# Performance work log

Measured on AMD Instinct MI355X. Metric: run time of the kernel, lower is better.

Reference implementation:

```python
import jax, jax.numpy as jnp
import numpy as np

KERNEL = 10   # kernel_size (asserted == 10 in the original)
HEADS = 4
BN_SCALE = 1.0 / np.sqrt(1.0 + 1e-5)  # eval-mode BatchNorm1d (running mean 0, var 1, affine 1/0)


def get_dct_matrix(N):
    k = np.arange(N)[:, None].astype(np.float64)
    i = np.arange(N)[None, :].astype(np.float64)
    w = np.full((N, 1), np.sqrt(2.0 / N))
    w[0, 0] = np.sqrt(1.0 / N)
    dct_m = w * np.cos(np.pi * (i + 0.5) * k / N)
    idct_m = np.linalg.inv(dct_m)
    return dct_m.astype(np.float32), idct_m.astype(np.float32)


def conv1d(x, w):  # x [B,C,L], w [O,I,K], valid, no bias
    return jax.lax.conv_general_dilated(x, w, (1,), 'VALID',
                                        dimension_numbers=('NCH', 'OIH', 'NCH'))


def conv_stack(x, w1, w2):  # Conv1d(k=6) -> ReLU -> Conv1d(k=5) -> ReLU
    return jax.nn.relu(conv1d(jax.nn.relu(conv1d(x, w1)), w2))


# vmap over the 4 heads' weights -> [H,B,D,L]
heads_conv = jax.vmap(conv_stack, in_axes=(None, 0, 0))


def _forward(src, cq1, cq2, ck1, ck2, lw, lb, giw, gia, gib, gbw, gba, gbb,
             gow, goa, gob, dct_n, output_n, input_n):
    bs, in_feat = src.shape[0], src.shape[2]
    src = src[:, :input_n]                                   # [B,50,48]
    src_key = jnp.swapaxes(src, 1, 2)[:, :, :input_n - output_n]  # [B,48,25]
    src_query = jnp.swapaxes(src, 1, 2)[:, :, -KERNEL:]           # [B,48,10]

    dct_np, idct_np = get_dct_matrix(KERNEL + output_n)
    dct_m = jnp.asarray(dct_np)
    idct_m = jnp.asarray(idct_np)

    vn = input_n - KERNEL - output_n + 1  # 16 overlapping value windows
    vl = KERNEL + output_n                # window length 35
    idx = np.arange(vl)[None, :] + np.arange(vn)[:, None]    # [16,35]
    windows = src[:, idx]                                    # [B,16,35,48]
    # DCT per window then flatten per-joint coeffs: [B,16,48*dct_n]
    val = jnp.einsum('dv,bnvf->bndf', dct_m[:dct_n], windows)
    src_value = jnp.swapaxes(val, 2, 3).reshape(bs, vn, -1)  # [B,16,480]

    key_h = heads_conv(src_key / 1000.0, ck1, ck2)           # [H,B,512,16]
    query_h = heads_conv(src_query / 1000.0, cq1, cq2)       # [H,B,512,1]

    # sum-normalized (non-softmax) attention
    score = jnp.einsum('hbdq,hbdk->hbqk', query_h, key_h) + 1e-15  # [H,B,1,16]
    att_w = score / jnp.sum(score, axis=3, keepdims=True)
    dct_att = jnp.einsum('hbk,bkf->hbf', att_w[:, :, 0], src_value)  # [H,B,480]
    dct_att = dct_att.reshape(HEADS, bs, in_feat, dct_n)
    att_cat = jnp.transpose(dct_att, (1, 0, 2, 3)).reshape(bs, HEADS * in_feat, dct_n)
    # Linear over the concatenated head/joint axis: [B,48,dct_n]
    att_lin = jnp.einsum('bmd,nm->bnd', att_cat, lw) + lb[None, :, None]

    # last kernel_size frames + last frame repeated output_n times
    gather_idx = np.concatenate([np.arange(input_n - KERNEL, input_n),
                                 np.full(output_n, input_n - 1)])
    input_gcn = src[:, gather_idx]                           # [B,35,48]
    dct_in = jnp.einsum('dv,bvf->bfd', dct_m[:dct_n], input_gcn)  # [B,48,10]
    dct_in = jnp.concatenate([dct_in, att_lin], axis=-1)     # [B,48,20]

    # GCN (Mao et al. style): learnable adjacency [48,48], eval-mode BN, tanh
    def gc(h, a, w, b):
        return jnp.einsum('nm,bmf->bnf', a, h @ w) + b

    y = jnp.tanh(gc(dct_in, gia, giw, gib) * BN_SCALE)       # [B,48,512]
    for s in range(gbw.shape[0]):
        r = y
        for j in range(2):
            y = jnp.tanh(gc(y, gba[s, j], gbw[s, j], gbb[s, j]) * BN_SCALE)
        y = y + r
    dct_out = gc(y, goa, gow, gob) + dct_in                  # [B,48,20]

    out_gcn = jnp.einsum('vd,bnd->bvn', idct_m[:, :dct_n], dct_out[:, :, :dct_n])  # [B,35,48]
    return out_gcn[:, :, None, :]                            # [B,35,itera=1,48]


def setup_inputs() -> dict:
    key = jax.random.key(0)
    ks = jax.random.split(key, 16)
    bs, in_feat, d_model, dct_n = 256, 48, 512, 10
    s = 0.05
    return {
        'src': jax.random.normal(ks[0], (bs, 50, in_feat), jnp.float32) * 1000.0,
        'convQ_w1': jax.random.normal(ks[1], (HEADS, d_model, in_feat, 6), jnp.float32) * s,
        'convQ_w2': jax.random.normal(ks[2], (HEADS, d_model, d_model, 5), jnp.float32) * s,
        'convK_w1': jax.random.normal(ks[3], (HEADS, d_model, in_feat, 6), jnp.float32) * s,
        'convK_w2': jax.random.normal(ks[4], (HEADS, d_model, d_model, 5), jnp.float32) * s,
        'linear_w': jax.random.normal(ks[5], (in_feat, HEADS * in_feat), jnp.float32) * s,
        'linear_b': jax.random.normal(ks[6], (in_feat,), jnp.float32) * s,
        'gc_in_w': jax.random.normal(ks[7], (2 * dct_n, d_model), jnp.float32) * s,
        'gc_in_att': jax.random.normal(ks[8], (in_feat, in_feat), jnp.float32) * s,
        'gc_in_b': jax.random.normal(ks[9], (d_model,), jnp.float32) * s,
        'gcb_w': jax.random.normal(ks[10], (2, 2, d_model, d_model), jnp.float32) * s,
        'gcb_att': jax.random.normal(ks[11], (2, 2, in_feat, in_feat), jnp.float32) * s,
        'gcb_b': jax.random.normal(ks[12], (2, 2, d_model), jnp.float32) * s,
        'gc_out_w': jax.random.normal(ks[13], (d_model, 2 * dct_n), jnp.float32) * s,
        'gc_out_att': jax.random.normal(ks[14], (in_feat, in_feat), jnp.float32) * s,
        'gc_out_b': jax.random.normal(ks[15], (2 * dct_n,), jnp.float32) * s,
        'dct_n': 10, 'output_n': 25, 'input_n': 50, 'itera': 1,
    }


def reference(src, convQ_w1, convQ_w2, convK_w1, convK_w2, linear_w, linear_b,
              gc_in_w, gc_in_att, gc_in_b, gcb_w, gcb_att, gcb_b,
              gc_out_w, gc_out_att, gc_out_b, dct_n, output_n, input_n, itera):
    # itera=1 path only (itera>1 in the original references undefined attrs)
    return _forward(src, convQ_w1, convQ_w2, convK_w1, convK_w2, linear_w, linear_b,
                    gc_in_w, gc_in_att, gc_in_b, gcb_w, gcb_att, gcb_b,
                    gc_out_w, gc_out_att, gc_out_b, dct_n, output_n, input_n)
```

## Files before the change

kernel.cpp:

```cpp
#include <hip/hip_runtime.h>
#include <math.h>

static constexpr float BN_SCALE_F = 0.9999950000374997f;

typedef __bf16 bf16;
typedef bf16 bf16x8 __attribute__((ext_vector_type(8)));
typedef bf16 bf16x4 __attribute__((ext_vector_type(4)));
typedef float floatx4 __attribute__((ext_vector_type(4)));

#define GLOBAL_AS __attribute__((address_space(1)))
#define LDS_AS __attribute__((address_space(3)))

__device__ __forceinline__ float tanh_fast(float x) {
    const float e = __expf(2.f * x);
    return 1.f - 2.f / (e + 1.f);
}

__device__ __forceinline__ void d_trw1(int id, const float* w, bf16* wt) {
    if (id < 4 * 512 * 320) {
        int ho = id / 320, c = id % 320;
        float v = (c < 288) ? w[(long)ho * 288 + (c % 48) * 6 + (c / 48)] * 1e-3f : 0.f;
        wt[id] = (bf16)v;
    }
}
__global__ __launch_bounds__(256) void k_prep(
    const float* __restrict__ src, const float* __restrict__ cq1,
    const float* __restrict__ ck1, const float* __restrict__ cq2,
    const float* __restrict__ ck2, const float* __restrict__ gbw,
    const float* __restrict__ giw, const float* __restrict__ gow,
    const float* __restrict__ gba, float* __restrict__ dct10,
    bf16* __restrict__ srcbf, bf16* __restrict__ w1tq, bf16* __restrict__ w1tk,
    bf16* __restrict__ w2tq, bf16* __restrict__ w2tk, bf16* __restrict__ gbwF,
    bf16* __restrict__ giwF, bf16* __restrict__ gowT, bf16* __restrict__ gbaP) {
    __shared__ float lds[4160];
    int bb = blockIdx.x;
    const int t = threadIdx.x;
    if (bb < 2) {
        int id = bb * 256 + t;
        if (id < 350) {
            int k = id / 35, i = id % 35;
            double w = (k == 0) ? sqrt(1.0 / 35.0) : sqrt(2.0 / 35.0);
            dct10[id] = (float)(w * cos(3.14159265358979323846 * (i + 0.5) * k / 35.0));
        }
        return;
    }
    bb -= 2;
    if (bb < 2401) {
        int id = bb * 256 + t;
        if (id < 614656) srcbf[id] = (bf16)(id < 614400 ? src[id] : 0.f);
        return;
    }
    bb -= 2401;
    if (bb < 2560) { d_trw1(bb * 256 + t, cq1, w1tq); return; }
    bb -= 2560;
    if (bb < 2560) { d_trw1(bb * 256 + t, ck1, w1tk); return; }
    bb -= 2560;
    if (bb < 4096) {
        const bool isQ = bb < 2048;
        const int ho = isQ ? bb : bb - 2048;
        const float* wrow = (isQ ? cq2 : ck2) + (long)ho * 2560;
        bf16* orow = (isQ ? w2tq : w2tk) + (long)ho * 2560;
        for (int j = t; j < 2560; j += 256) lds[j] = wrow[j];
        __syncthreads();
        for (int c = t; c < 2560; c += 256) {
            const int k = c >> 9, ii = c & 511;
            orow[c] = (bf16)lds[ii * 5 + k];
        }
        return;
    }
    bb -= 4096;
    if (bb < 256) {
        const int l = bb >> 6, tile = bb & 63;
        const int tr = tile >> 3, tc = tile & 7;
        const float* in = gbw + (long)l * 262144;
        bf16* o = gbwF + (long)l * 262144;
#pragma unroll
        for (int r = 0; r < 16; ++r) {
            const int kl = (t >> 6) * 16 + r, ml = t & 63;
            lds[kl * 65 + ml] = in[(long)(tr * 64 + kl) * 512 + tc * 64 + ml];
        }
        __syncthreads();
        for (int j = t; j < 4096; j += 256) {
            const int q = j >> 9, r4 = j & 511;
            const int gl = q >> 2, sl = (q >> 1) & 1, jt = q & 1;
            const int lane = r4 >> 3, e = r4 & 7;
            const int fr = lane & 15, fq = lane >> 4;
            const int kk = sl * 32 + fq * 8 + e;
            const int ff = gl * 32 + jt * 16 + fr;
            o[(long)(tc * 2 + gl) * 16384 + (long)(tr * 2 + sl) * 1024 + jt * 512 + r4] =
                (bf16)lds[kk * 65 + ff];
        }
        return;
    }
    bb -= 256;
    if (bb < 128) {
        int id = bb * 256 + t;
        if (id < 32768) {
            const int r2 = id & 2047;
            const int s = r2 >> 10, r3 = r2 & 1023;
            const int jt = r3 >> 9, r4 = r3 & 511;
            const int lane = r4 >> 3, e = r4 & 7;
            const int fr = lane & 15, fq = lane >> 4;
            const int g = id >> 11;
            const int k = s * 32 + fq * 8 + e;
            const int f = g * 32 + jt * 16 + fr;
            giwF[id] = (bf16)(k < 20 ? giw[k * 512 + f] : 0.f);
        }
        return;
    }
    bb -= 128;
    if (bb < 64) {
        int id = bb * 256 + t;
        int d = id >> 9, k = id & 511;
        gowT[id] = (bf16)(d < 20 ? gow[k * 20 + d] : 0.f);
        return;
    }
    bb -= 64;
    {
        int id = bb * 256 + t;
        if (id < 12288) {
            int l = id / 3072, r = id % 3072, n = r >> 6, m = r & 63;
            gbaP[id] = (bf16)(m < 48 ? gba[l * 2304 + n * 48 + m] : 0.f);
        }
    }
}

__global__ __launch_bounds__(256) void k_conv1(
    const bf16* __restrict__ w1tk, const bf16* __restrict__ w1tq,
    const bf16* __restrict__ srcbf, bf16* __restrict__ r1k,
    bf16* __restrict__ r1q) {
    int bx, by, bz;
    const bf16* A;
    bf16* C;
    int NT, toff;
    long cStr;
    {
        const int i = blockIdx.x;
        if (i < 1280) {
            bz = i / 320;
            const int r = i % 320;
            bx = r % 40;
            by = r / 40;
            A = w1tk; C = r1k; NT = 20; toff = 0; cStr = 2621440L;
        } else {
            const int j = i - 1280;
            bz = j / 80;
            const int r = j % 80;
            bx = r % 10;
            by = r / 10;
            A = w1tq; C = r1q; NT = 5; toff = 40; cStr = 655360L;
        }
    }
    __shared__ bf16 As[64 * 64];
    __shared__ bf16 Bs[128 * 64];
    const int tid = threadIdx.x;
    const int wave = tid >> 6;
    const int lane = tid & 63;
    const int wm = (wave & 1) * 32;
    const int wn = (wave >> 1) * 64;
    const int m0 = by * 64;
    const int n0 = bx * 128;
    A += (long)bz * (512L * 320);

    const int srow = lane >> 3;
    const int gch = (lane & 7) ^ srow;
    const bf16* aptr[2];
    const bf16* bptr[4];
#pragma unroll
    for (int i = 0; i < 2; ++i) {
        const int ar = wave * 16 + i * 8 + srow;
        aptr[i] = A + (long)(m0 + ar) * 320 + gch * 8;
    }
#pragma unroll
    for (int i = 0; i < 4; ++i) {
        const int ar = wave * 32 + i * 8 + srow;
        const int n = n0 + ar;
        const long bbase = (long)(n / NT) * 2400 + (long)((n % NT) + toff) * 48;
        bptr[i] = srcbf + bbase + gch * 8;
    }

    floatx4 acc[4][2];
#pragma unroll
    for (int j = 0; j < 4; ++j)
#pragma unroll
        for (int i = 0; i < 2; ++i) acc[j][i] = (floatx4){0.f, 0.f, 0.f, 0.f};

    const int fr = lane & 15;
    const int fq = lane >> 4;
    const int fx = lane & 7;

    for (int k0 = 0; k0 < 320; k0 += 64) {
#pragma unroll
        for (int i = 0; i < 2; ++i)
            __builtin_amdgcn_global_load_lds(
                (const GLOBAL_AS void*)(aptr[i] + k0),
                (LDS_AS void*)(As + (wave * 16 + i * 8) * 64), 16, 0, 0);
#pragma unroll
        for (int i = 0; i < 4; ++i)
            __builtin_amdgcn_global_load_lds(
                (const GLOBAL_AS void*)(bptr[i] + k0),
                (LDS_AS void*)(Bs + (wave * 32 + i * 8) * 64), 16, 0, 0);
        __syncthreads();
#pragma unroll
        for (int kk = 0; kk < 2; ++kk) {
            bf16x8 af[2], bfr[4];
#pragma unroll
            for (int im = 0; im < 2; ++im)
                af[im] = *(const bf16x8*)(As + (wm + im * 16 + fr) * 64 +
                                          ((((kk << 2) + fq) ^ fx) << 3));
#pragma unroll
            for (int in = 0; in < 4; ++in)
                bfr[in] = *(const bf16x8*)(Bs + (wn + in * 16 + fr) * 64 +
                                           ((((kk << 2) + fq) ^ fx) << 3));
#pragma unroll
            for (int in = 0; in < 4; ++in)
#pragma unroll
                for (int im = 0; im < 2; ++im)
                    acc[in][im] = __builtin_amdgcn_mfma_f32_16x16x32_bf16(
                        af[im], bfr[in], acc[in][im], 0, 0, 0);
        }
        __syncthreads();
    }
#pragma unroll
    for (int in = 0; in < 4; ++in) {
        const long n = n0 + wn + in * 16 + fr;
#pragma unroll
        for (int im = 0; im < 2; ++im) {
            floatx4 v = acc[in][im];
            const long m = m0 + wm + im * 16 + (fq << 2);
            v.x = fmaxf(v.x, 0.f);
            v.y = fmaxf(v.y, 0.f);
            v.z = fmaxf(v.z, 0.f);
            v.w = fmaxf(v.w, 0.f);
            bf16* Cp = C + (long)bz * cStr + n * 512 + m;
            bf16x4 ov;
            ov[0] = (bf16)v.x;
            ov[1] = (bf16)v.y;
            ov[2] = (bf16)v.z;
            ov[3] = (bf16)v.w;
            *(bf16x4*)Cp = ov;
        }
    }
}

__global__ __launch_bounds__(256) void k_conv2(
    const bf16* __restrict__ w2tk, const bf16* __restrict__ r1k,
    bf16* __restrict__ keyh, const bf16* __restrict__ w2tq,
    const bf16* __restrict__ r1q, bf16* __restrict__ qh) {
    const int K = 2560;
    int bx, by, bz;
    const bf16 *A, *B;
    bf16* C;
    bool kMode;
    long aStr, bStr, cStr;
    {
        const int i = blockIdx.x;
        if (i < 1024) {
            const int slot = i & 7;
            bz = slot >> 1;
            const int half = slot & 1;
            const int j = i >> 3;
            bx = half * 16 + (j & 15);
            by = j >> 4;
            A = w2tk; B = r1k; C = keyh; kMode = true;
            aStr = 512L * 2560; bStr = 2621440L; cStr = 2097152L;
        } else {
            const int j = i - 1024;
            bz = j >> 4;
            const int r = j & 15;
            bx = r & 1;
            by = r >> 1;
            A = w2tq; B = r1q; C = qh; kMode = false;
            aStr = 512L * 2560; bStr = 655360L; cStr = 131072L;
        }
    }
    __shared__ bf16 As[64 * 64];
    __shared__ bf16 Bs[160 * 64];
    const int tid = threadIdx.x;
    const int wave = tid >> 6;
    const int lane = tid & 63;
    const int wm = (wave & 1) * 32;
    const int wn = (wave >> 1) * 64;
    const int m0 = by * 64;
    const int n0 = bx * 128;
    A += (long)bz * aStr;
    B += (long)bz * bStr;

    const int srow = lane >> 3;
    const int gch = (lane & 7) ^ srow;
    const bf16* aptr[2];
#pragma unroll
    for (int i = 0; i < 2; ++i) {
        const int ar = wave * 16 + i * 8 + srow;
        aptr[i] = A + (long)(m0 + ar) * K + gch * 8;
    }

    floatx4 acc[4][2];
#pragma unroll
    for (int j = 0; j < 4; ++j)
#pragma unroll
        for (int i = 0; i < 2; ++i) acc[j][i] = (floatx4){0.f, 0.f, 0.f, 0.f};

    const int fr = lane & 15;
    const int fq = lane >> 4;
    const int fx = lane & 7;

    if (kMode) {
        const bf16* bptrK[5];
        int ldsBK[5];
#pragma unroll
        for (int j = 0; j < 5; ++j) {
            const int rloc = wave * 40 + j * 8 + srow;
            const int brel = rloc / 20, pos = rloc % 20;
            bptrK[j] = B + ((long)((bx * 8 + brel) * 20 + pos)) * 512 +
                       ((lane & 7) ^ (pos & 7)) * 8;
            ldsBK[j] = rloc * 64 + (lane & 7) * 8;
        }
        const int bq = wn >> 4;
        for (int c0i = 0; c0i < 8; ++c0i) {
            const int c0 = c0i * 64;
#pragma unroll
            for (int w = 0; w < 5; ++w) {
                const int k0 = w * 512 + c0;
#pragma unroll
                for (int i = 0; i < 2; ++i)
                    __builtin_amdgcn_global_load_lds(
                        (const GLOBAL_AS void*)(aptr[i] + k0),
                        (LDS_AS void*)(As + (wave * 16 + i * 8) * 64), 16, 0, 0);
                if (w == 0) {
#pragma unroll
                    for (int j = 0; j < 5; ++j)
                        __builtin_amdgcn_global_load_lds(
                            (const GLOBAL_AS void*)(bptrK[j] + c0),
                            (LDS_AS void*)(Bs + ldsBK[j]), 16, 0, 0);
                }
                __syncthreads();
#pragma unroll
                for (int kk = 0; kk < 2; ++kk) {
                    bf16x8 af[2], bfr[4];
#pragma unroll
                    for (int im = 0; im < 2; ++im)
                        af[im] = *(const bf16x8*)(As + (wm + im * 16 + fr) * 64 +
                                                  ((((kk << 2) + fq) ^ fx) << 3));
#pragma unroll
                    for (int nt = 0; nt < 4; ++nt) {
                        const int row = (bq + nt) * 20 + fr + w;
                        bfr[nt] = *(const bf16x8*)(
                            Bs + row * 64 +
                            ((((kk << 2) + fq) ^ ((fr + w) & 7)) << 3));
                    }
#pragma unroll
                    for (int nt = 0; nt < 4; ++nt)
#pragma unroll
                        for (int im = 0; im < 2; ++im)
                            acc[nt][im] = __builtin_amdgcn_mfma_f32_16x16x32_bf16(
                                af[im], bfr[nt], acc[nt][im], 0, 0, 0);
                }
                __syncthreads();
            }
        }
    } else {
        const bf16* bptr[4];
#pragma unroll
        for (int i = 0; i < 4; ++i) {
            const int ar = wave * 32 + i * 8 + srow;
            bptr[i] = B + (long)(n0 + ar) * K + gch * 8;
        }
        for (int k0 = 0; k0 < K; k0 += 64) {
#pragma unroll
            for (int i = 0; i < 2; ++i)
                __builtin_amdgcn_global_load_lds(
                    (const GLOBAL_AS void*)(aptr[i] + k0),
                    (LDS_AS void*)(As + (wave * 16 + i * 8) * 64), 16, 0, 0);
#pragma unroll
            for (int i = 0; i < 4; ++i)
                __builtin_amdgcn_global_load_lds(
                    (const GLOBAL_AS void*)(bptr[i] + k0),
                    (LDS_AS void*)(Bs + (wave * 32 + i * 8) * 64), 16, 0, 0);
            __syncthreads();
#pragma unroll
            for (int kk = 0; kk < 2; ++kk) {
                bf16x8 af[2], bfr[4];
#pragma unroll
                for (int im = 0; im < 2; ++im)
                    af[im] = *(const bf16x8*)(As + (wm + im * 16 + fr) * 64 +
                                              ((((kk << 2) + fq) ^ fx) << 3));
#pragma unroll
                for (int in = 0; in < 4; ++in)
                    bfr[in] = *(const bf16x8*)(Bs + (wn + in * 16 + fr) * 64 +
                                               ((((kk << 2) + fq) ^ fx) << 3));
#pragma unroll
                for (int in = 0; in < 4; ++in)
#pragma unroll
                    for (int im = 0; im < 2; ++im)
                        acc[in][im] = __builtin_amdgcn_mfma_f32_16x16x32_bf16(
                            af[im], bfr[in], acc[in][im], 0, 0, 0);
            }
            __syncthreads();
        }
    }
#pragma unroll
    for (int in = 0; in < 4; ++in) {
        const long n = n0 + wn + in * 16 + fr;
#pragma unroll
        for (int im = 0; im < 2; ++im) {
            floatx4 v = acc[in][im];
            const long m = m0 + wm + im * 16 + (fq << 2);
            v.x = fmaxf(v.x, 0.f);
            v.y = fmaxf(v.y, 0.f);
            v.z = fmaxf(v.z, 0.f);
            v.w = fmaxf(v.w, 0.f);
            bf16* Cp = C + (long)bz * cStr + n * 512 + m;
            bf16x4 ov;
            ov[0] = (bf16)v.x;
            ov[1] = (bf16)v.y;
            ov[2] = (bf16)v.z;
            ov[3] = (bf16)v.w;
            *(bf16x4*)Cp = ov;
        }
    }
}

__global__ __launch_bounds__(512) void k_att(
    const bf16* __restrict__ qh, const bf16* __restrict__ keyh,
    const float* __restrict__ src, const float* __restrict__ dct10,
    const float* __restrict__ lw, const float* __restrict__ lb,
    const float* __restrict__ gia, float* __restrict__ dctin,
    bf16* __restrict__ z0) {
    const int b = blockIdx.x;
    const int t = threadIdx.x;
    __shared__ float BIG[9216];
    __shared__ float WD[2400];
    __shared__ float D[350];
    __shared__ float L[1920];
    __shared__ float dinS[960];
    __shared__ float sS[64];
    __shared__ float awS[64];

    {
        const int g = t >> 3, lane = t & 7;
        const int h = g >> 4, tt = g & 15;
        const bf16* q = qh + ((long)h * 256 + b) * 512 + lane * 64;
        const bf16* kr = keyh + (long)h * 2097152 + ((long)b * 16 + tt) * 512 + lane * 64;
        float p = 0.f;
#pragma unroll
        for (int i = 0; i < 8; ++i) {
            const bf16x8 qv = *(const bf16x8*)(q + i * 8);
            const bf16x8 kv = *(const bf16x8*)(kr + i * 8);
#pragma unroll
            for (int j = 0; j < 8; ++j) p = fmaf((float)qv[j], (float)kv[j], p);
        }
        p += __shfl_down(p, 4, 8);
        p += __shfl_down(p, 2, 8);
        p += __shfl_down(p, 1, 8);
        if (lane == 0) sS[g] = p + 1e-15f;
    }
    for (int i = t; i < 2400; i += 512) WD[i] = src[(long)b * 2400 + i];
    for (int i = t; i < 350; i += 512) D[i] = dct10[i];
    __syncthreads();
    if (t < 4) {
        float s = 0.f;
#pragma unroll
        for (int k = 0; k < 16; ++k) s += sS[t * 16 + k];
        const float inv = 1.f / s;
#pragma unroll
        for (int k = 0; k < 16; ++k) awS[t * 16 + k] = sS[t * 16 + k] * inv;
    }
    __syncthreads();
    if (t < 480) {
        const int f = t / 10, d = t % 10;
        float dreg[35];
#pragma unroll
        for (int v = 0; v < 35; ++v) dreg[v] = D[d * 35 + v];
#pragma unroll 2
        for (int n = 0; n < 16; ++n) {
            float acc = 0.f;
#pragma unroll
            for (int v = 0; v < 35; ++v)
                acc = fmaf(dreg[v], WD[(n + v) * 48 + f], acc);
            BIG[n * 480 + t] = acc;
        }
        float acc = 0.f;
#pragma unroll
        for (int v = 0; v < 10; ++v)
            acc = fmaf(dreg[v], WD[(40 + v) * 48 + f], acc);
        float cs = 0.f;
#pragma unroll
        for (int v = 10; v < 35; ++v) cs += dreg[v];
        acc = fmaf(cs, WD[49 * 48 + f], acc);
        dinS[f * 20 + d] = acc;
        dctin[(long)b * 960 + f * 20 + d] = acc;
    }
    __syncthreads();
    for (int p = 0; p < 4; ++p) {
        const int idx = t + p * 512;
        if (idx < 1920) {
            const int h = idx / 480, j = idx % 480;
            float acc = 0.f;
#pragma unroll
            for (int k = 0; k < 16; ++k)
                acc = fmaf(awS[h * 16 + k], BIG[k * 480 + j], acc);
            L[idx] = acc;
        }
    }
    __syncthreads();
    for (int i = t; i < 9216; i += 512) BIG[i] = lw[i];
    for (int i = t; i < 2304; i += 512) WD[i] = gia[i];
    __syncthreads();
    if (t < 480) {
        const int n = t / 10, d = t % 10;
        float acc = lb[n];
#pragma unroll
        for (int h = 0; h < 4; ++h)
#pragma unroll
            for (int f = 0; f < 48; ++f)
                acc = fmaf(BIG[n * 192 + h * 48 + f], L[h * 480 + f * 10 + d], acc);
        dinS[n * 20 + 10 + d] = acc;
        dctin[(long)b * 960 + n * 20 + 10 + d] = acc;
    }
    __syncthreads();
    for (int p = 0; p < 2; ++p) {
        const int idx = t + p * 512;
        if (idx < 960) {
            const int n = idx / 20, d = idx % 20;
            float acc = 0.f;
#pragma unroll
            for (int m = 0; m < 48; ++m)
                acc = fmaf(WD[n * 48 + m], dinS[m * 20 + d], acc);
            z0[((long)b * 48 + n) * 64 + d] = (bf16)acc;
        }
    }
    for (int i = t; i < 2112; i += 512) {
        const int n = i / 44, c = 20 + i % 44;
        z0[((long)b * 48 + n) * 64 + c] = (bf16)0.f;
    }
}

template <bool TOUT, int S>
__device__ __forceinline__ void gcn_matmul3(
    const bf16* __restrict__ zSrc, const bf16* __restrict__ Wf,
    const float* __restrict__ bias, const bf16* __restrict__ resT,
    bf16* __restrict__ outS, const int wave, const int lane) {
    const int fr = lane & 15, fq = lane >> 4;
    const int f0 = wave * 32;
    floatx4 acc[3][2];
#pragma unroll
    for (int it = 0; it < 3; ++it)
#pragma unroll
        for (int jt = 0; jt < 2; ++jt) acc[it][jt] = (floatx4){0.f, 0.f, 0.f, 0.f};
    const bf16* wp = Wf + (long)wave * (S * 1024) + (lane << 3);
    bf16x8 w0[4], w1[4];
    constexpr int PRE = (S < 3) ? S : 3;
#pragma unroll
    for (int s = 0; s < PRE; ++s) {
        w0[s] = *(const bf16x8*)(wp + s * 1024);
        w1[s] = *(const bf16x8*)(wp + s * 1024 + 512);
    }
#pragma unroll
    for (int s = 0; s < S; ++s) {
        bf16x8 af[3];
#pragma unroll
        for (int it = 0; it < 3; ++it)
            af[it] = *(const bf16x8*)(zSrc + (it * 16 + fr) * 520 + s * 32 + fq * 8);
        if (s + 3 < S) {
            const int ns = (s + 3) & 3;
            w0[ns] = *(const bf16x8*)(wp + (s + 3) * 1024);
            w1[ns] = *(const bf16x8*)(wp + (s + 3) * 1024 + 512);
        }
        const int sl = s & 3;
#pragma unroll
        for (int it = 0; it < 3; ++it) {
            acc[it][0] = __builtin_amdgcn_mfma_f32_16x16x32_bf16(af[it], w0[sl],
                                                                acc[it][0], 0, 0, 0);
            acc[it][1] = __builtin_amdgcn_mfma_f32_16x16x32_bf16(af[it], w1[sl],
                                                                acc[it][1], 0, 0, 0);
        }
    }
#pragma unroll
    for (int jt = 0; jt < 2; ++jt) {
        const int f = f0 + jt * 16 + fr;
        const float bv = bias[f];
#pragma unroll
        for (int it = 0; it < 3; ++it) {
            const int ir0 = it * 16 + fq * 4;
            float v[4];
#pragma unroll
            for (int r = 0; r < 4; ++r)
                v[r] = tanh_fast((acc[it][jt][r] + bv) * BN_SCALE_F);
            if (resT) {
                const bf16x4 rv = *(const bf16x4*)(resT + f * 48 + ir0);
#pragma unroll
                for (int r = 0; r < 4; ++r) v[r] += (float)rv[r];
            }
            if (TOUT) {
                bf16x4 ov;
#pragma unroll
                for (int r = 0; r < 4; ++r) ov[r] = (bf16)v[r];
                *(bf16x4*)(outS + f * 48 + ir0) = ov;
            } else {
#pragma unroll
                for (int r = 0; r < 4; ++r)
                    outS[(ir0 + r) * 520 + f] = (bf16)v[r];
            }
        }
    }
}

__device__ __forceinline__ void gcn_attmul2(const bf16* __restrict__ gA,
                                            const bf16* __restrict__ YinT,
                                            bf16* __restrict__ zOut,
                                            const int wave, const int lane) {
    const int fr = lane & 15, fq = lane >> 4;
    const int f0 = wave * 32;
    floatx4 acc[3][2];
#pragma unroll
    for (int it = 0; it < 3; ++it)
#pragma unroll
        for (int jt = 0; jt < 2; ++jt) acc[it][jt] = (floatx4){0.f, 0.f, 0.f, 0.f};
    bf16x8 af0[3], af1[3], bv0[2], bv1[2];
#pragma unroll
    for (int it = 0; it < 3; ++it) {
        af0[it] = *(const bf16x8*)(gA + (it * 16 + fr) * 64 + fq * 8);
        af1[it] = *(const bf16x8*)(gA + (it * 16 + fr) * 64 + 32 + fq * 8);
    }
#pragma unroll
    for (int jt = 0; jt < 2; ++jt) {
        const int f = f0 + jt * 16 + fr;
        bv0[jt] = *(const bf16x8*)(YinT + f * 48 + fq * 8);
        bv1[jt] = *(const bf16x8*)(YinT + f * 48 + 32 + fq * 8);
    }
#pragma unroll
    for (int it = 0; it < 3; ++it)
#pragma unroll
        for (int jt = 0; jt < 2; ++jt) {
            acc[it][jt] = __builtin_amdgcn_mfma_f32_16x16x32_bf16(af0[it], bv0[jt],
                                                                 acc[it][jt], 0, 0, 0);
            acc[it][jt] = __builtin_amdgcn_mfma_f32_16x16x32_bf16(af1[it], bv1[jt],
                                                                 acc[it][jt], 0, 0, 0);
        }
#pragma unroll
    for (int jt = 0; jt < 2; ++jt) {
        const int f = f0 + jt * 16 + fr;
#pragma unroll
        for (int it = 0; it < 3; ++it)
#pragma unroll
            for (int r = 0; r < 4; ++r)
                zOut[(it * 16 + fq * 4 + r) * 520 + f] = (bf16)acc[it][jt][r];
    }
}

__global__ __launch_bounds__(1024) void k_gcn(
    const bf16* __restrict__ z0, const bf16* __restrict__ giwF,
    const float* __restrict__ gib, const bf16* __restrict__ gbwF,
    const bf16* __restrict__ gbaP, const float* __restrict__ gbb,
    const float* __restrict__ goa, const bf16* __restrict__ gowT,
    const float* __restrict__ gob, const float* __restrict__ dctin,
    const float* __restrict__ dct10, float* __restrict__ out) {
    const int b = blockIdx.x;
    const int t = threadIdx.x;
    const int wave = t >> 6, lane = t & 63;
    __shared__ __align__(16) bf16 yaS[24976];
    __shared__ __align__(16) bf16 ybS[24592];
    __shared__ __align__(16) bf16 zS[48 * 520];

    if (t < 384) {
        const int r = t >> 3, c = t & 7;
        *(bf16x8*)(zS + r * 520 + c * 8) =
            *(const bf16x8*)(z0 + ((long)b * 48 + r) * 64 + c * 8);
    } else if (t < 400) {
        yaS[24576 + (t - 384)] = (bf16)0.f;
    } else if (t < 416) {
        ybS[24576 + (t - 400)] = (bf16)0.f;
    }
    __syncthreads();
    gcn_matmul3<true, 2>(zS, giwF, gib, nullptr, yaS, wave, lane);
    __syncthreads();

#pragma unroll
    for (int l = 0; l < 4; ++l) {
        const bf16* YinT = (l == 0 || l == 3) ? yaS : ybS;
        gcn_attmul2(gbaP + l * 3072, YinT, zS, wave, lane);
        __syncthreads();
        const bf16* Res = (l == 1) ? yaS : (l == 3 ? ybS : nullptr);
        if (l < 3)
            gcn_matmul3<true, 16>(zS, gbwF + (long)l * 262144, gbb + l * 512,
                                  Res, (l < 2) ? ybS : yaS, wave, lane);
        else
            gcn_matmul3<false, 16>(zS, gbwF + 3L * 262144, gbb + 3 * 512, Res,
                                   yaS, wave, lane);
        __syncthreads();
    }
    float* T2 = (float*)ybS;
    float* dS = ((float*)ybS) + 960;
    float* goaS = ((float*)ybS) + 1920;
    float* Df = ((float*)ybS) + 4224;
    if (t < 384) {
        const int fr2 = lane & 15, fq2 = lane >> 4;
        const int it = wave >> 1, jt = wave & 1;
        floatx4 accT = (floatx4){0.f, 0.f, 0.f, 0.f};
        const bf16* ap = yaS + (it * 16 + fr2) * 520 + fq2 * 8;
        const bf16* gp = gowT + (long)(jt * 16 + fr2) * 512 + fq2 * 8;
        for (int k0 = 0; k0 < 512; k0 += 32) {
            const bf16x8 av = *(const bf16x8*)(ap + k0);
            const bf16x8 gv = *(const bf16x8*)(gp + k0);
            accT = __builtin_amdgcn_mfma_f32_16x16x32_bf16(av, gv, accT, 0, 0, 0);
        }
        const int d = jt * 16 + fr2;
        if (d < 20) {
#pragma unroll
            for (int r = 0; r < 4; ++r) {
                const int m = it * 16 + fq2 * 4 + r;
                T2[m * 20 + d] = accT[r];
            }
        }
    } else {
        for (int i = t - 384; i < 2304; i += 640) goaS[i] = goa[i];
        for (int i = t - 384; i < 350; i += 640) Df[i] = dct10[i];
    }
    __syncthreads();
    if (t < 960) {
        const int n = t / 20, d = t % 20;
        float acc = gob[d] + dctin[(long)b * 960 + t];
#pragma unroll
        for (int m = 0; m < 48; ++m)
            acc = fmaf(goaS[n * 48 + m], T2[m * 20 + d], acc);
        dS[t] = acc;
    }
    __syncthreads();
    for (int e = t; e < 1680; e += 1024) {
        const int v = e / 48, n = e % 48;
        float acc = 0.f;
#pragma unroll
        for (int d = 0; d < 10; ++d)
            acc = fmaf(Df[d * 35 + v], dS[n * 20 + d], acc);
        out[(long)b * 1680 + e] = acc;
    }
}

static constexpr size_t WS_DCT10 = 0;
static constexpr size_t WS_ATTW = 1536;
static constexpr size_t WS_QH = WS_ATTW + 65536;
static constexpr size_t WS_DCTIN = WS_QH + 2097152;
static constexpr size_t WS_DCTOUT = WS_DCTIN + 983040;
static constexpr size_t WS_SRCVAL = WS_DCTOUT + 983040;
static constexpr size_t WS_PAD0 = WS_SRCVAL + 7864320;
static constexpr size_t WS_GOWT = WS_PAD0;
static constexpr size_t WS_GBAP = WS_PAD0 + 32768;
static constexpr size_t WS_SRCBF = WS_PAD0 + 8388608;
static constexpr size_t WS_W1TQ = WS_SRCBF + 1229824;
static constexpr size_t WS_W1TK = WS_W1TQ + 1310720;
static constexpr size_t WS_W2TQ = WS_W1TK + 1310720;
static constexpr size_t WS_W2TK = WS_W2TQ + 10485760;
static constexpr size_t WS_GBWT = WS_W2TK + 10485760;
static constexpr size_t WS_R1K = WS_GBWT + 2097152;
static constexpr size_t WS_R1Q = WS_R1K + 20971520;
static constexpr size_t WS_T = WS_R1Q + 5242880;
static constexpr size_t WS_GIWP = WS_T + 50331648;
static constexpr size_t WS_KEYH = WS_T;
static constexpr size_t WS_Z0 = WS_T + 17825792;

extern "C" void kernel_launch(void* const* d_in, const int* in_sizes, int n_in,
                              void* d_out, int out_size, void* d_ws,
                              size_t ws_size, hipStream_t stream) {
    const float* src = (const float*)d_in[0];
    const float* cq1 = (const float*)d_in[1];
    const float* cq2 = (const float*)d_in[2];
    const float* ck1 = (const float*)d_in[3];
    const float* ck2 = (const float*)d_in[4];
    const float* lw = (const float*)d_in[5];
    const float* lb = (const float*)d_in[6];
    const float* giw = (const float*)d_in[7];
    const float* gia = (const float*)d_in[8];
    const float* gib = (const float*)d_in[9];
    const float* gbw = (const float*)d_in[10];
    const float* gba = (const float*)d_in[11];
    const float* gbb = (const float*)d_in[12];
    const float* gow = (const float*)d_in[13];
    const float* goa = (const float*)d_in[14];
    const float* gob = (const float*)d_in[15];
    float* out = (float*)d_out;
    char* ws = (char*)d_ws;

    float* dct10 = (float*)(ws + WS_DCT10);
    bf16* qh = (bf16*)(ws + WS_QH);
    float* dctin = (float*)(ws + WS_DCTIN);
    bf16* keyh = (bf16*)(ws + WS_KEYH);
    bf16* srcbf = (bf16*)(ws + WS_SRCBF);
    bf16* w1tq = (bf16*)(ws + WS_W1TQ);
    bf16* w1tk = (bf16*)(ws + WS_W1TK);
    bf16* w2tq = (bf16*)(ws + WS_W2TQ);
    bf16* w2tk = (bf16*)(ws + WS_W2TK);
    bf16* gbwF = (bf16*)(ws + WS_GBWT);
    bf16* r1k = (bf16*)(ws + WS_R1K);
    bf16* r1q = (bf16*)(ws + WS_R1Q);
    bf16* giwF = (bf16*)(ws + WS_GIWP);
    bf16* gowT = (bf16*)(ws + WS_GOWT);
    bf16* gbaP = (bf16*)(ws + WS_GBAP);
    bf16* z0 = (bf16*)(ws + WS_Z0);

    k_prep<<<12115, 256, 0, stream>>>(src, cq1, ck1, cq2, ck2, gbw, giw, gow,
                                      gba, dct10, srcbf, w1tq, w1tk, w2tq,
                                      w2tk, gbwF, giwF, gowT, gbaP);

    k_conv1<<<1600, 256, 0, stream>>>(w1tk, w1tq, srcbf, r1k, r1q);

    k_conv2<<<1088, 256, 0, stream>>>(w2tk, r1k, keyh, w2tq, r1q, qh);

    k_att<<<256, 512, 0, stream>>>(qh, keyh, src, dct10, lw, lb, gia, dctin, z0);

    k_gcn<<<256, 1024, 0, stream>>>(z0, giwF, gib, gbwF, gbaP, gbb, goa, gowT,
                                    gob, dctin, dct10, out);
}
```

Baseline: 302.9 us.

## Fuse attention kernel into GCN kernel, keeping intermediates in shared memory

Merges the attention/DCT kernel into the GCN kernel, so each batch block computes the attention scores, the DCT inputs and z0 directly into LDS, reusing the GCN's yaS/ybS buffers as scratch. This removes one kernel launch and the global round-trips of z0 and dctin. Work is respread from 512 to 1024 threads, splitting the window-DCT loop in half per thread. The trade-off is a larger, more serialized single kernel with only 256 blocks and heavy LDS use.

```diff
diff --git a/kernel.cpp b/kernel.cpp
--- a/kernel.cpp
+++ b/kernel.cpp
@@ -421,121 +421,6 @@
     }
 }
 
-__global__ __launch_bounds__(512) void k_att(
-    const bf16* __restrict__ qh, const bf16* __restrict__ keyh,
-    const float* __restrict__ src, const float* __restrict__ dct10,
-    const float* __restrict__ lw, const float* __restrict__ lb,
-    const float* __restrict__ gia, float* __restrict__ dctin,
-    bf16* __restrict__ z0) {
-    const int b = blockIdx.x;
-    const int t = threadIdx.x;
-    __shared__ float BIG[9216];
-    __shared__ float WD[2400];
-    __shared__ float D[350];
-    __shared__ float L[1920];
-    __shared__ float dinS[960];
-    __shared__ float sS[64];
-    __shared__ float awS[64];
-
-    {
-        const int g = t >> 3, lane = t & 7;
-        const int h = g >> 4, tt = g & 15;
-        const bf16* q = qh + ((long)h * 256 + b) * 512 + lane * 64;
-        const bf16* kr = keyh + (long)h * 2097152 + ((long)b * 16 + tt) * 512 + lane * 64;
-        float p = 0.f;
-#pragma unroll
-        for (int i = 0; i < 8; ++i) {
-            const bf16x8 qv = *(const bf16x8*)(q + i * 8);
-            const bf16x8 kv = *(const bf16x8*)(kr + i * 8);
-#pragma unroll
-            for (int j = 0; j < 8; ++j) p = fmaf((float)qv[j], (float)kv[j], p);
-        }
-        p += __shfl_down(p, 4, 8);
-        p += __shfl_down(p, 2, 8);
-        p += __shfl_down(p, 1, 8);
-        if (lane == 0) sS[g] = p + 1e-15f;
-    }
-    for (int i = t; i < 2400; i += 512) WD[i] = src[(long)b * 2400 + i];
-    for (int i = t; i < 350; i += 512) D[i] = dct10[i];
-    __syncthreads();
-    if (t < 4) {
-        float s = 0.f;
-#pragma unroll
-        for (int k = 0; k < 16; ++k) s += sS[t * 16 + k];
-        const float inv = 1.f / s;
-#pragma unroll
-        for (int k = 0; k < 16; ++k) awS[t * 16 + k] = sS[t * 16 + k] * inv;
-    }
-    __syncthreads();
-    if (t < 480) {
-        const int f = t / 10, d = t % 10;
-        float dreg[35];
-#pragma unroll
-        for (int v = 0; v < 35; ++v) dreg[v] = D[d * 35 + v];
-#pragma unroll 2
-        for (int n = 0; n < 16; ++n) {
-            float acc = 0.f;
-#pragma unroll
-            for (int v = 0; v < 35; ++v)
-                acc = fmaf(dreg[v], WD[(n + v) * 48 + f], acc);
-            BIG[n * 480 + t] = acc;
-        }
-        float acc = 0.f;
-#pragma unroll
-        for (int v = 0; v < 10; ++v)
-            acc = fmaf(dreg[v], WD[(40 + v) * 48 + f], acc);
-        float cs = 0.f;
-#pragma unroll
-        for (int v = 10; v < 35; ++v) cs += dreg[v];
-        acc = fmaf(cs, WD[49 * 48 + f], acc);
-        dinS[f * 20 + d] = acc;
-        dctin[(long)b * 960 + f * 20 + d] = acc;
-    }
-    __syncthreads();
-    for (int p = 0; p < 4; ++p) {
-        const int idx = t + p * 512;
-        if (idx < 1920) {
-            const int h = idx / 480, j = idx % 480;
-            float acc = 0.f;
-#pragma unroll
-            for (int k = 0; k < 16; ++k)
-                acc = fmaf(awS[h * 16 + k], BIG[k * 480 + j], acc);
-            L[idx] = acc;
-        }
-    }
-    __syncthreads();
-    for (int i = t; i < 9216; i += 512) BIG[i] = lw[i];
-    for (int i = t; i < 2304; i += 512) WD[i] = gia[i];
-    __syncthreads();
-    if (t < 480) {
-        const int n = t / 10, d = t % 10;
-        float acc = lb[n];
-#pragma unroll
-        for (int h = 0; h < 4; ++h)
-#pragma unroll
-            for (int f = 0; f < 48; ++f)
-                acc = fmaf(BIG[n * 192 + h * 48 + f], L[h * 480 + f * 10 + d], acc);
-        dinS[n * 20 + 10 + d] = acc;
-        dctin[(long)b * 960 + n * 20 + 10 + d] = acc;
-    }
-    __syncthreads();
-    for (int p = 0; p < 2; ++p) {
-        const int idx = t + p * 512;
-        if (idx < 960) {
-            const int n = idx / 20, d = idx % 20;
-            float acc = 0.f;
-#pragma unroll
-            for (int m = 0; m < 48; ++m)
-                acc = fmaf(WD[n * 48 + m], dinS[m * 20 + d], acc);
-            z0[((long)b * 48 + n) * 64 + d] = (bf16)acc;
-        }
-    }
-    for (int i = t; i < 2112; i += 512) {
-        const int n = i / 44, c = 20 + i % 44;
-        z0[((long)b * 48 + n) * 64 + c] = (bf16)0.f;
-    }
-}
-
 template <bool TOUT, int S>
 __device__ __forceinline__ void gcn_matmul3(
     const bf16* __restrict__ zSrc, const bf16* __restrict__ Wf,
@@ -649,33 +534,131 @@
     }
 }
 
-__global__ __launch_bounds__(1024) void k_gcn(
-    const bf16* __restrict__ z0, const bf16* __restrict__ giwF,
+__global__ __launch_bounds__(1024) void k_attgcn(
+    const bf16* __restrict__ qh, const bf16* __restrict__ keyh,
+    const float* __restrict__ src, const float* __restrict__ dct10,
+    const float* __restrict__ lw, const float* __restrict__ lb,
+    const float* __restrict__ gia, const bf16* __restrict__ giwF,
     const float* __restrict__ gib, const bf16* __restrict__ gbwF,
     const bf16* __restrict__ gbaP, const float* __restrict__ gbb,
     const float* __restrict__ goa, const bf16* __restrict__ gowT,
-    const float* __restrict__ gob, const float* __restrict__ dctin,
-    const float* __restrict__ dct10, float* __restrict__ out) {
+    const float* __restrict__ gob, float* __restrict__ out) {
     const int b = blockIdx.x;
     const int t = threadIdx.x;
     const int wave = t >> 6, lane = t & 63;
     __shared__ __align__(16) bf16 yaS[24976];
     __shared__ __align__(16) bf16 ybS[24592];
     __shared__ __align__(16) bf16 zS[48 * 520];
-
-    if (t < 384) {
-        const int r = t >> 3, c = t & 7;
-        *(bf16x8*)(zS + r * 520 + c * 8) =
-            *(const bf16x8*)(z0 + ((long)b * 48 + r) * 64 + c * 8);
-    } else if (t < 400) {
-        yaS[24576 + (t - 384)] = (bf16)0.f;
-    } else if (t < 416) {
-        ybS[24576 + (t - 400)] = (bf16)0.f;
+    __shared__ float dinS[960];
+
+    float* BIG = (float*)yaS;
+    float* WD = (float*)ybS;
+    float* D = WD + 2400;
+    float* L = D + 350;
+    float* sS = L + 1920;
+    float* awS = sS + 64;
+
+    {
+        const int g = t >> 4, l16 = t & 15;
+        const int h = g >> 4, tt = g & 15;
+        const bf16* q = qh + ((long)h * 256 + b) * 512 + l16 * 32;
+        const bf16* kr = keyh + (long)h * 2097152 + ((long)b * 16 + tt) * 512 + l16 * 32;
+        float p = 0.f;
+#pragma unroll
+        for (int i = 0; i < 4; ++i) {
+            const bf16x8 qv = *(const bf16x8*)(q + i * 8);
+            const bf16x8 kv = *(const bf16x8*)(kr + i * 8);
+#pragma unroll
+            for (int j = 0; j < 8; ++j) p = fmaf((float)qv[j], (float)kv[j], p);
+        }
+        p += __shfl_down(p, 8, 16);
+        p += __shfl_down(p, 4, 16);
+        p += __shfl_down(p, 2, 16);
+        p += __shfl_down(p, 1, 16);
+        if (l16 == 0) sS[g] = p + 1e-15f;
+    }
+    for (int i = t; i < 2400; i += 1024) WD[i] = src[(long)b * 2400 + i];
+    for (int i = t; i < 350; i += 1024) D[i] = dct10[i];
+    __syncthreads();
+    if (t < 4) {
+        float s = 0.f;
+#pragma unroll
+        for (int k = 0; k < 16; ++k) s += sS[t * 16 + k];
+        const float inv = 1.f / s;
+#pragma unroll
+        for (int k = 0; k < 16; ++k) awS[t * 16 + k] = sS[t * 16 + k] * inv;
+    }
+    __syncthreads();
+    if (t < 960) {
+        const int p2 = t >> 1, half = t & 1;
+        const int f = p2 / 10, d = p2 % 10;
+        float dreg[35];
+#pragma unroll
+        for (int v = 0; v < 35; ++v) dreg[v] = D[d * 35 + v];
+        const int nlo = half * 8;
+#pragma unroll 2
+        for (int n = nlo; n < nlo + 8; ++n) {
+            float acc = 0.f;
+#pragma unroll
+            for (int v = 0; v < 35; ++v)
+                acc = fmaf(dreg[v], WD[(n + v) * 48 + f], acc);
+            BIG[n * 480 + p2] = acc;
+        }
+        if (half == 0) {
+            float acc = 0.f;
+#pragma unroll
+            for (int v = 0; v < 10; ++v)
+                acc = fmaf(dreg[v], WD[(40 + v) * 48 + f], acc);
+            float cs = 0.f;
+#pragma unroll
+            for (int v = 10; v < 35; ++v) cs += dreg[v];
+            acc = fmaf(cs, WD[49 * 48 + f], acc);
+            dinS[f * 20 + d] = acc;
+        }
+    }
+    __syncthreads();
+    for (int idx = t; idx < 1920; idx += 1024) {
+        const int h = idx / 480, j = idx % 480;
+        float acc = 0.f;
+#pragma unroll
+        for (int k = 0; k < 16; ++k)
+            acc = fmaf(awS[h * 16 + k], BIG[k * 480 + j], acc);
+        L[idx] = acc;
+    }
+    __syncthreads();
+    for (int i = t; i < 9216; i += 1024) BIG[i] = lw[i];
+    for (int i = t; i < 2304; i += 1024) WD[i] = gia[i];
+    __syncthreads();
+    if (t < 480) {
+        const int n = t / 10, d = t % 10;
+        float acc = lb[n];
+#pragma unroll
+        for (int h = 0; h < 4; ++h)
+#pragma unroll
+            for (int f = 0; f < 48; ++f)
+                acc = fmaf(BIG[n * 192 + h * 48 + f], L[h * 480 + f * 10 + d], acc);
+        dinS[n * 20 + 10 + d] = acc;
+    }
+    __syncthreads();
+    if (t < 960) {
+        const int n = t / 20, d = t % 20;
+        float acc = 0.f;
+#pragma unroll
+        for (int m = 0; m < 48; ++m)
+            acc = fmaf(WD[n * 48 + m], dinS[m * 20 + d], acc);
+        zS[n * 520 + d] = (bf16)acc;
+    } else if (t < 976) {
+        yaS[24576 + (t - 960)] = (bf16)0.f;
+    } else if (t < 992) {
+        ybS[24576 + (t - 976)] = (bf16)0.f;
+    }
+    for (int i = t; i < 2112; i += 1024) {
+        const int n = i / 44, c = 20 + i % 44;
+        zS[n * 520 + c] = (bf16)0.f;
     }
     __syncthreads();
     gcn_matmul3<true, 2>(zS, giwF, gib, nullptr, yaS, wave, lane);
     __syncthreads();
-
 #pragma unroll
     for (int l = 0; l < 4; ++l) {
         const bf16* YinT = (l == 0 || l == 3) ? yaS : ybS;
@@ -720,7 +703,7 @@
     __syncthreads();
     if (t < 960) {
         const int n = t / 20, d = t % 20;
-        float acc = gob[d] + dctin[(long)b * 960 + t];
+        float acc = gob[d] + dinS[t];
 #pragma unroll
         for (int m = 0; m < 48; ++m)
             acc = fmaf(goaS[n * 48 + m], T2[m * 20 + d], acc);
@@ -757,7 +740,6 @@
 static constexpr size_t WS_T = WS_R1Q + 5242880;
 static constexpr size_t WS_GIWP = WS_T + 50331648;
 static constexpr size_t WS_KEYH = WS_T;
-static constexpr size_t WS_Z0 = WS_T + 17825792;
 
 extern "C" void kernel_launch(void* const* d_in, const int* in_sizes, int n_in,
                               void* d_out, int out_size, void* d_ws,
@@ -783,7 +765,6 @@
 
     float* dct10 = (float*)(ws + WS_DCT10);
     bf16* qh = (bf16*)(ws + WS_QH);
-    float* dctin = (float*)(ws + WS_DCTIN);
     bf16* keyh = (bf16*)(ws + WS_KEYH);
     bf16* srcbf = (bf16*)(ws + WS_SRCBF);
     bf16* w1tq = (bf16*)(ws + WS_W1TQ);
@@ -796,7 +777,6 @@
     bf16* giwF = (bf16*)(ws + WS_GIWP);
     bf16* gowT = (bf16*)(ws + WS_GOWT);
     bf16* gbaP = (bf16*)(ws + WS_GBAP);
-    bf16* z0 = (bf16*)(ws + WS_Z0);
 
     k_prep<<<12115, 256, 0, stream>>>(src, cq1, ck1, cq2, ck2, gbw, giw, gow,
                                       gba, dct10, srcbf, w1tq, w1tk, w2tq,
@@ -806,8 +786,7 @@
 
     k_conv2<<<1088, 256, 0, stream>>>(w2tk, r1k, keyh, w2tq, r1q, qh);
 
-    k_att<<<256, 512, 0, stream>>>(qh, keyh, src, dct10, lw, lb, gia, dctin, z0);
-
-    k_gcn<<<256, 1024, 0, stream>>>(z0, giwF, gib, gbwF, gbaP, gbb, goa, gowT,
-                                    gob, dctin, dct10, out);
-}
+    k_attgcn<<<256, 1024, 0, stream>>>(qh, keyh, src, dct10, lw, lb, gia,
+                                       giwF, gib, gbwF, gbaP, gbb, goa, gowT,
+                                       gob, out);
+}
```

After: 375.2 us. 1.24x slower.
